# Optimization experiments

Hardware: AMD Instinct MI355X
Metric: run time of the kernel (lower is better)

The kernel has to match this reference:

```python
import jax, jax.numpy as jnp
import numpy as np

H = 4096      # hidden_size
NH = 32       # num_heads
QR = 1536     # q_lora_rank
KVR = 512     # kv_lora_rank
RD = 64       # qk_rope_head_dim
ND = 128      # qk_nope_head_dim
VD = 128      # v_head_dim
QK = RD + ND  # qk_head_dim
EPS = 1e-6
THETA = 10000.0
B, S = 2, 1024


def rmsnorm(x, w):
    # torch: x / (||x|| * d^-0.5 + eps) * w
    norm = jnp.sqrt(jnp.sum(x * x, axis=-1, keepdims=True)) * (x.shape[-1] ** -0.5)
    return x / (norm + EPS) * w


def rope_cos_sin(seq_len):
    inv_freq = 1.0 / (THETA ** (jnp.arange(0, RD, 2, dtype=jnp.float32) / RD))
    t = jnp.arange(seq_len, dtype=jnp.float32)
    freqs = jnp.outer(t, inv_freq)              # [S, RD/2]
    emb = jnp.concatenate([freqs, freqs], -1)   # [S, RD]
    return jnp.cos(emb), jnpp_cos_sin_dummy() if False else jnp.sin(emb)


def rotate_half(x):
    x1, x2 = jnp.split(x, 2, axis=-1)
    return jnp.concatenate([-x2, x1], axis=-1)


def setup_inputs() -> dict:
    key = jax.random.key(0)
    ks = jax.random.split(key, 8)
    sc = 0.02
    return {
        "hidden_states": jax.random.normal(ks[0], (B, S, H), jnp.float32),
        "w_qa": jax.random.normal(ks[1], (H, QR), jnp.float32) * sc,
        "g_qa": jnp.ones((QR,), jnp.float32),
        "w_qb": jax.random.normal(ks[2], (QR, NH * QK), jnp.float32) * sc,
        "w_kva": jax.random.normal(ks[3], (H, KVR + RD), jnp.float32) * sc,
        "g_kva": jnp.ones((KVR,), jnp.float32),
        "w_kvb": jax.random.normal(ks[4], (KVR, NH * (ND + VD)), jnp.float32) * sc,
        "w_o": jax.random.normal(ks[5], (NH * VD, H), jnp.float32) * sc,
    }


def reference(hidden_states, w_qa, g_qa, w_qb, w_kva, g_kva, w_kvb, w_o):
    b, s, _ = hidden_states.shape
    # Q path: LoRA down -> RMSNorm -> LoRA up
    q_c = rmsnorm(hidden_states @ w_qa, g_qa)                       # [b,s,QR]
    q = (q_c @ w_qb).reshape(b, s, NH, QK).transpose(0, 2, 1, 3)    # [b,NH,s,QK]
    q_nope, q_rope = q[..., :ND], q[..., ND:]
    # KV path: joint down-proj, split compressed kv and rope key
    kv = hidden_states @ w_kva                                      # [b,s,KVR+RD]
    k_c, k_rope = kv[..., :KVR], kv[..., KVR:]
    k_c = rmsnorm(k_c, g_kva)
    kst = (k_c @ w_kvb).reshape(b, s, NH, ND + VD).transpose(0, 2, 1, 3)
    k_nope, v = kst[..., :ND], kst[..., ND:]                        # [b,NH,s,ND],[b,NH,s,VD]
    # partial RoPE on the rope slice only
    inv_freq = 1.0 / (THETA ** (jnp.arange(0, RD, 2, dtype=jnp.float32) / RD))
    freqs = jnp.outer(jnp.arange(s, dtype=jnp.float32), inv_freq)
    emb = jnp.concatenate([freqs, freqs], -1)                       # [s,RD]
    cos = jnp.cos(emb)[None, None]                                  # [1,1,s,RD]
    sin = jnp.sin(emb)[None, None]
    k_rope = k_rope[:, None]                                        # [b,1,s,RD]
    q_rope = q_rope * cos + rotate_half(q_rope) * sin
    k_rope = k_rope * cos + rotate_half(k_rope) * sin
    k_rope = jnp.broadcast_to(k_rope, (b, NH, s, RD))
    query = jnp.concatenate([q_nope, q_rope], -1)                   # [b,NH,s,QK]
    key_s = jnp.concatenate([k_nope, k_rope], -1)
    scaling = QK ** -0.5
    scores = jnp.einsum("bhqd,bhkd->bhqk", query, key_s) * scaling  # [b,NH,s,s]
    attn = jax.nn.softmax(scores, axis=-1)
    out = jnp.einsum("bhqk,bhkd->bhqd", attn, v)                    # [b,NH,s,VD]
    out = out.transpose(0, 2, 1, 3).reshape(b, s, NH * VD)
    return out @ w_o                                                # [b,s,H]
```

## Files before the change

### kernel.cpp

```cpp
#include <hip/hip_runtime.h>
#include <hip/hip_bf16.h>
#include <stdint.h>
#include <string.h>

typedef float f32x4_t __attribute__((ext_vector_type(4)));
typedef short s16x8_t __attribute__((ext_vector_type(8)));

#define LDS_AS __attribute__((address_space(3)))
#define GLB_AS __attribute__((address_space(1)))

__device__ __forceinline__ void gload16(void* lds, const void* g) {
    __builtin_amdgcn_global_load_lds((const GLB_AS uint32_t*)g,
                                     (LDS_AS uint32_t*)lds, 16, 0, 0);
}

__device__ __forceinline__ uint32_t pack_bf16(float lo, float hi) {
    union { __hip_bfloat16 h; uint16_t u; } a, b;
    a.h = __float2bfloat16(lo); b.h = __float2bfloat16(hi);
    return (uint32_t)a.u | ((uint32_t)b.u << 16);
}

__global__ __launch_bounds__(256) void rope_table_kernel(float* __restrict__ cos_t,
                                                         float* __restrict__ sin_t) {
    int idx = blockIdx.x * 256 + threadIdx.x;
    int s = idx >> 6, j = idx & 63;
    float invf = powf(10000.0f, -((float)((j & 31) * 2)) / 64.0f);
    float a = (float)s * invf;
    cos_t[idx] = cosf(a);
    sin_t[idx] = sinf(a);
}

__global__ __launch_bounds__(256) void f32_to_bf16_kernel(const float* __restrict__ in,
                                                          __hip_bfloat16* __restrict__ out, int n4) {
    int i = blockIdx.x * 256 + threadIdx.x;
    if (i >= n4) return;
    float4 v = reinterpret_cast<const float4*>(in)[i];
    struct __align__(8) BF4 { __hip_bfloat16 a, b, c, d; } r;
    r.a = __float2bfloat16(v.x); r.b = __float2bfloat16(v.y);
    r.c = __float2bfloat16(v.z); r.d = __float2bfloat16(v.w);
    reinterpret_cast<BF4*>(out)[i] = r;
}

__global__ __launch_bounds__(256) void transpose_convert(const float* __restrict__ W,
                                                         __hip_bfloat16* __restrict__ WT,
                                                         int K, int N, int Npad, float scale) {
    __shared__ float tile[32][33];
    int k0 = blockIdx.y * 32, n0 = blockIdx.x * 32;
    int tx = threadIdx.x & 31, ty = threadIdx.x >> 5;
#pragma unroll
    for (int i = 0; i < 4; i++) {
        int ky = i * 8 + ty;
        int n = n0 + tx;
        float v = 0.f;
        if (n < N) v = W[(size_t)(k0 + ky) * N + n];
        tile[ky][tx] = v;
    }
    __syncthreads();
#pragma unroll
    for (int i = 0; i < 4; i++) {
        int ny = i * 8 + ty;
        WT[(size_t)(n0 + ny) * K + k0 + tx] = __float2bfloat16(tile[tx][ny] * scale);
    }
}

__global__ __launch_bounds__(256) void rmsnorm_kernel(const float* __restrict__ in,
                                                      const float* __restrict__ g,
                                                      __hip_bfloat16* __restrict__ out,
                                                      int cols, int in_stride) {
    int row = blockIdx.x;
    const float* x = in + (size_t)row * in_stride;
    float ss = 0.f;
    for (int c = threadIdx.x; c < cols; c += 256) { float v = x[c]; ss += v * v; }
#pragma unroll
    for (int off = 32; off > 0; off >>= 1) ss += __shfl_xor(ss, off);
    __shared__ float red[4];
    if ((threadIdx.x & 63) == 0) red[threadIdx.x >> 6] = ss;
    __syncthreads();
    float tot = red[0] + red[1] + red[2] + red[3];
    float rms = sqrtf(tot / (float)cols);
    float inv = 1.0f / (rms + 1e-6f);
    for (int c = threadIdx.x; c < cols; c += 256)
        out[(size_t)row * cols + c] = __float2bfloat16(x[c] * inv * g[c]);
}

__global__ __launch_bounds__(256) void rope_k_kernel(const float* __restrict__ kv,
                                                     const float* __restrict__ cos_t,
                                                     const float* __restrict__ sin_t,
                                                     __hip_bfloat16* __restrict__ k_rope) {
    int idx = blockIdx.x * 256 + threadIdx.x;
    int tok = idx >> 5, j = idx & 31;
    int s = tok & 1023;
    const float* x = kv + (size_t)tok * 640 + 512;
    float x1 = x[j], x2 = x[j + 32];
    float co = cos_t[s * 64 + j], si = sin_t[s * 64 + j];
    __hip_bfloat16* o = k_rope + (size_t)tok * 64;
    o[j]      = __float2bfloat16(x1 * co - x2 * si);
    o[j + 32] = __float2bfloat16(x2 * co + x1 * si);
}

__global__ __launch_bounds__(256) void rope_q_kernel(__hip_bfloat16* __restrict__ q,
                                                     const float* __restrict__ cos_t,
                                                     const float* __restrict__ sin_t) {
    int tok = blockIdx.x;
    int s = tok & 1023;
    __hip_bfloat16* row = q + (size_t)tok * 6144;
#pragma unroll
    for (int it = 0; it < 4; it++) {
        int i = it * 256 + threadIdx.x;
        int h = i >> 5, j = i & 31;
        int c = h * 192 + 128 + j;
        float x1 = __bfloat162float(row[c]), x2 = __bfloat162float(row[c + 32]);
        float co = cos_t[s * 64 + j], si = sin_t[s * 64 + j];
        row[c]      = __float2bfloat16(x1 * co - x2 * si);
        row[c + 32] = __float2bfloat16(x2 * co + x1 * si);
    }
}

__global__ __launch_bounds__(256) void transpose_v_kernel(const __hip_bfloat16* __restrict__ kst,
                                                          __hip_bfloat16* __restrict__ V_T) {
    __shared__ __hip_bfloat16 t[64][136];
    int bid = blockIdx.x;
    int st = bid & 15, bh = bid >> 4;
    int h = bh & 31, b = bh >> 5;
    int s0 = st * 64;
#pragma unroll
    for (int i = 0; i < 4; i++) {
        int c = i * 256 + threadIdx.x;
        int r = c >> 4, oct = c & 15;
        *(s16x8_t*)&t[r][oct * 8] =
            *(const s16x8_t*)&kst[(size_t)(b * 1024 + s0 + r) * 8192 + h * 256 + 128 + oct * 8];
    }
    __syncthreads();
#pragma unroll
    for (int i = 0; i < 4; i++) {
        int c = i * 256 + threadIdx.x;
        int vd = c >> 3, oct = c & 7;
        s16x8_t pk;
#pragma unroll
        for (int e = 0; e < 8; e++) pk[e] = *(const short*)&t[oct * 8 + e][vd];
        *(s16x8_t*)&V_T[((size_t)bh * 128 + vd) * 1024 + s0 + oct * 8] = pk;
    }
}

template <int MODE>
__global__ __launch_bounds__(256, 2) void gemm_bt_128(const __hip_bfloat16* __restrict__ A,
                                                      const __hip_bfloat16* __restrict__ BT,
                                                      void* __restrict__ Cout, void* __restrict__ C1,
                                                      int M, int N, int K, int N0, int N1) {
    __shared__ __hip_bfloat16 As[128 * 64];
    __shared__ __hip_bfloat16 Bs[128 * 64];
    const int tid = threadIdx.x;
    const int l = tid & 63, w = tid >> 6;
    const int wr = w >> 1, wc = w & 1;
    const int m0 = blockIdx.y * 128, n0 = blockIdx.x * 128;
    const int lrow = l & 15, lkg = l >> 4;

    f32x4_t acc[4][4];
#pragma unroll
    for (int i = 0; i < 4; i++)
#pragma unroll
        for (int j = 0; j < 4; j++) acc[i][j] = (f32x4_t){0.f, 0.f, 0.f, 0.f};

    for (int k0 = 0; k0 < K; k0 += 64) {
        __syncthreads();
#pragma unroll
        for (int i = 0; i < 4; i++) {
            int s = i * 256 + tid;
            int row = s >> 3, po = s & 7;
            int lo = po ^ (row & 7);
            gload16(&As[s * 8], &A[(size_t)(m0 + row) * K + k0 + lo * 8]);
            gload16(&Bs[s * 8], &BT[(size_t)(n0 + row) * K + k0 + lo * 8]);
        }
        __syncthreads();
#pragma unroll
        for (int ks = 0; ks < 2; ks++) {
            s16x8_t a[4], b[4];
#pragma unroll
            for (int m = 0; m < 4; m++) {
                int row = wr * 64 + m * 16 + lrow;
                int oct = (ks * 4 + lkg) ^ (row & 7);
                a[m] = *(const s16x8_t*)&As[row * 64 + oct * 8];
            }
#pragma unroll
            for (int n = 0; n < 4; n++) {
                int row = wc * 64 + n * 16 + lrow;
                int oct = (ks * 4 + lkg) ^ (row & 7);
                b[n] = *(const s16x8_t*)&Bs[row * 64 + oct * 8];
            }
#pragma unroll
            for (int m = 0; m < 4; m++)
#pragma unroll
                for (int n = 0; n < 4; n++)
                    acc[m][n] = __builtin_amdgcn_mfma_f32_16x16x32_bf16(a[m], b[n], acc[m][n], 0, 0, 0);
        }
    }
#pragma unroll
    for (int m = 0; m < 4; m++) {
        int row = m0 + wr * 64 + m * 16 + lkg * 4;
#pragma unroll
        for (int n = 0; n < 4; n++) {
            int col = n0 + wc * 64 + n * 16 + lrow;
#pragma unroll
            for (int r = 0; r < 4; r++) {
                float v = acc[m][n][r];
                if (MODE == 1) {
                    ((__hip_bfloat16*)Cout)[(size_t)(row + r) * N + col] = __float2bfloat16(v);
                } else if (MODE == 0) {
                    ((float*)Cout)[(size_t)(row + r) * N + col] = v;
                } else {
                    if (col < N0) ((float*)Cout)[(size_t)(row + r) * N0 + col] = v;
                    else          ((float*)C1)[(size_t)(row + r) * N1 + (col - N0)] = v;
                }
            }
        }
    }
}

__global__ __launch_bounds__(256, 3) void attn8_kernel(const __hip_bfloat16* __restrict__ q,
                                                       const __hip_bfloat16* __restrict__ kst,
                                                       const __hip_bfloat16* __restrict__ k_rope,
                                                       const __hip_bfloat16* __restrict__ V_T,
                                                       __hip_bfloat16* __restrict__ attn_out) {
    __shared__ __align__(16) __hip_bfloat16 Ks[2][64 * 192];

    int i = blockIdx.x;
    int bh = (i & 7) * 8 + ((i >> 3) & 7);
    int qt = i >> 6;
    int h = bh & 31, b = bh >> 5;
    int q0 = qt * 64;
    int tid = threadIdx.x, l = tid & 63, w = tid >> 6;
    int lrow = l & 15, lkg = l >> 4;

    s16x8_t qa[6];
    {
        size_t qbase = (size_t)(b * 1024 + q0 + w * 16 + lrow) * 6144 + h * 192;
#pragma unroll
        for (int f = 0; f < 6; f++)
            qa[f] = *(const s16x8_t*)&q[qbase + f * 32 + lkg * 8];
    }
    f32x4_t acc_o[8];
#pragma unroll
    for (int n = 0; n < 8; n++) acc_o[n] = (f32x4_t){0.f, 0.f, 0.f, 0.f};
    float m_run = -1e30f, l_run = 0.f;

    size_t krow_base = (size_t)(b * 1024) * 8192 + h * 256;
    size_t rrow_base = (size_t)(b * 1024) * 64;
    const __hip_bfloat16* vbase = V_T + (size_t)bh * 128 * 1024 + (size_t)lrow * 1024 + lkg * 8;

    auto stage_k = [&](int kv0, int buf) {
#pragma unroll
        for (int it = 0; it < 6; it++) {
            int s = it * 256 + tid;
            int row = s / 24, po = s - row * 24;
            int lo = po ^ (row & 7);
            const __hip_bfloat16* src = (lo < 16)
                ? &kst[krow_base + (size_t)(kv0 + row) * 8192 + lo * 8]
                : &k_rope[rrow_base + (size_t)(kv0 + row) * 64 + (lo - 16) * 8];
            gload16(&Ks[buf][s * 8], src);
        }
    };

    stage_k(0, 0);
    asm volatile("s_waitcnt vmcnt(0)" ::: "memory");
    __syncthreads();

    const int src0 = lrow + ((lkg & 1) << 5);
    const int src1 = src0 + 16;
    const bool hiC = (lkg >> 1) != 0;

    int cur = 0;
    for (int kt = 0; kt < 16; kt++) {
        int kv0 = kt * 64;

        if (kt < 15) stage_k(kv0 + 64, cur ^ 1);

        f32x4_t sc[4];
#pragma unroll
        for (int c = 0; c < 4; c++) sc[c] = (f32x4_t){0.f, 0.f, 0.f, 0.f};
        __builtin_amdgcn_s_setprio(1);
#pragma unroll
        for (int c = 0; c < 4; c++) {
            int row = c * 16 + lrow;
#pragma unroll
            for (int f = 0; f < 6; f++) {
                int po = ((f * 4 + lkg) ^ (lrow & 7)) * 8;
                s16x8_t kb = *(const s16x8_t*)&Ks[cur][row * 192 + po];
                sc[c] = __builtin_amdgcn_mfma_f32_16x16x32_bf16(kb, qa[f], sc[c], 0, 0, 0);
            }
        }
        __builtin_amdgcn_s_setprio(0);

        s16x8_t vb0[8];
#pragma unroll
        for (int n = 0; n < 8; n++)
            vb0[n] = *(const s16x8_t*)&vbase[(size_t)(n * 16) * 1024 + kv0];
        __builtin_amdgcn_sched_barrier(0);

        float mx = sc[0][0];
#pragma unroll
        for (int c = 0; c < 4; c++)
#pragma unroll
            for (int r = 0; r < 4; r++) mx = fmaxf(mx, sc[c][r]);
        mx = fmaxf(mx, __shfl_xor(mx, 16));
        mx = fmaxf(mx, __shfl_xor(mx, 32));
        if (!__all(mx - m_run <= 8.0f)) {
            float mn = fmaxf(m_run, mx);
            float al = __expf(m_run - mn);
            m_run = mn;
            l_run *= al;
#pragma unroll
            for (int n = 0; n < 8; n++) acc_o[n] *= al;
        }
        uint32_t u[4][2];
        float sum = 0.f;
#pragma unroll
        for (int c = 0; c < 4; c++) {
            float p0 = __expf(sc[c][0] - m_run), p1 = __expf(sc[c][1] - m_run);
            float p2 = __expf(sc[c][2] - m_run), p3 = __expf(sc[c][3] - m_run);
            sum += (p0 + p1) + (p2 + p3);
            u[c][0] = pack_bf16(p0, p1);
            u[c][1] = pack_bf16(p2, p3);
        }
        sum += __shfl_xor(sum, 16);
        sum += __shfl_xor(sum, 32);
        l_run += sum;

        {
            uint32_t a0 = __shfl((int)u[0][0], src0), b0 = __shfl((int)u[1][0], src0);
            uint32_t a1 = __shfl((int)u[0][1], src0), b1 = __shfl((int)u[1][1], src0);
            uint32_t a2 = __shfl((int)u[0][0], src1), b2 = __shfl((int)u[1][0], src1);
            uint32_t a3 = __shfl((int)u[0][1], src1), b3 = __shfl((int)u[1][1], src1);
            union { uint32_t wd[4]; s16x8_t v; } pb;
            pb.wd[0] = hiC ? b0 : a0;
            pb.wd[1] = hiC ? b1 : a1;
            pb.wd[2] = hiC ? b2 : a2;
            pb.wd[3] = hiC ? b3 : a3;
            __builtin_amdgcn_s_setprio(1);
#pragma unroll
            for (int n = 0; n < 8; n++)
                acc_o[n] = __builtin_amdgcn_mfma_f32_16x16x32_bf16(vb0[n], pb.v, acc_o[n], 0, 0, 0);
            __builtin_amdgcn_s_setprio(0);
        }
        s16x8_t vb1[8];
#pragma unroll
        for (int n = 0; n < 8; n++)
            vb1[n] = *(const s16x8_t*)&vbase[(size_t)(n * 16) * 1024 + kv0 + 32];
        {
            uint32_t a0 = __shfl((int)u[2][0], src0), b0 = __shfl((int)u[3][0], src0);
            uint32_t a1 = __shfl((int)u[2][1], src0), b1 = __shfl((int)u[3][1], src0);
            uint32_t a2 = __shfl((int)u[2][0], src1), b2 = __shfl((int)u[3][0], src1);
            uint32_t a3 = __shfl((int)u[2][1], src1), b3 = __shfl((int)u[3][1], src1);
            union { uint32_t wd[4]; s16x8_t v; } pb;
            pb.wd[0] = hiC ? b0 : a0;
            pb.wd[1] = hiC ? b1 : a1;
            pb.wd[2] = hiC ? b2 : a2;
            pb.wd[3] = hiC ? b3 : a3;
            __builtin_amdgcn_s_setprio(1);
#pragma unroll
            for (int n = 0; n < 8; n++)
                acc_o[n] = __builtin_amdgcn_mfma_f32_16x16x32_bf16(vb1[n], pb.v, acc_o[n], 0, 0, 0);
            __builtin_amdgcn_s_setprio(0);
        }

        asm volatile("s_waitcnt vmcnt(0)" ::: "memory");
        __syncthreads();
        cur ^= 1;
    }

    float inv = 1.0f / l_run;
    __hip_bfloat16* Ob = &Ks[0][0] + (size_t)w * (16 * 136);
#pragma unroll
    for (int n = 0; n < 8; n++) {
        uint32_t lo = pack_bf16(acc_o[n][0] * inv, acc_o[n][1] * inv);
        uint32_t hi = pack_bf16(acc_o[n][2] * inv, acc_o[n][3] * inv);
        uint32_t* dst = (uint32_t*)&Ob[lrow * 136 + n * 16 + lkg * 4];
        dst[0] = lo;
        dst[1] = hi;
    }
    asm volatile("s_waitcnt lgkmcnt(0)" ::: "memory");
    __builtin_amdgcn_sched_barrier(0);
#pragma unroll
    for (int it = 0; it < 4; it++) {
        int tr = it * 4 + lkg;
        s16x8_t ov = *(const s16x8_t*)&Ob[tr * 136 + lrow * 8];
        *(s16x8_t*)&attn_out[(size_t)(b * 1024 + q0 + w * 16 + tr) * 4096 + h * 128 + lrow * 8] = ov;
    }
}

extern "C" void kernel_launch(void* const* d_in, const int* in_sizes, int n_in,
                              void* d_out, int out_size, void* d_ws, size_t ws_size,
                              hipStream_t stream) {
    const float* hidden = (const float*)d_in[0];
    const float* w_qa   = (const float*)d_in[1];
    const float* g_qa   = (const float*)d_in[2];
    const float* w_qb   = (const float*)d_in[3];
    const float* w_kva  = (const float*)d_in[4];
    const float* g_kva  = (const float*)d_in[5];
    const float* w_kvb  = (const float*)d_in[6];
    const float* w_o    = (const float*)d_in[7];
    float* out = (float*)d_out;

    char* base = (char*)d_ws;
    size_t off = 0;
    auto alloc = [&](size_t bytes) -> void* {
        off = (off + 255) & ~(size_t)255;
        void* p = base + off;
        off += bytes;
        return p;
    };
    float* cos_t = (float*)alloc(1024 * 64 * 4);
    float* sin_t = (float*)alloc(1024 * 64 * 4);
    __hip_bfloat16* hid_b  = (__hip_bfloat16*)alloc(2048ull * 4096 * 2);
    __hip_bfloat16* wqaT   = (__hip_bfloat16*)alloc(1536ull * 4096 * 2);
    __hip_bfloat16* wkvaT  = (__hip_bfloat16*)alloc(640ull * 4096 * 2);
    __hip_bfloat16* wqbT   = (__hip_bfloat16*)alloc(6144ull * 1536 * 2);
    __hip_bfloat16* wkvbT  = (__hip_bfloat16*)alloc(8192ull * 512 * 2);
    __hip_bfloat16* woT    = (__hip_bfloat16*)alloc(4096ull * 4096 * 2);
    float* q_a             = (float*)alloc(2048ull * 1536 * 4);
    __hip_bfloat16* q_c    = (__hip_bfloat16*)alloc(2048ull * 1536 * 2);
    __hip_bfloat16* q_buf  = (__hip_bfloat16*)alloc(2048ull * 6144 * 2);
    float* kv              = (float*)alloc(2048ull * 640 * 4);
    __hip_bfloat16* k_c    = (__hip_bfloat16*)alloc(2048ull * 512 * 2);
    __hip_bfloat16* k_rope = (__hip_bfloat16*)alloc(2048ull * 64 * 2);
    __hip_bfloat16* kst    = (__hip_bfloat16*)alloc(2048ull * 8192 * 2);
    __hip_bfloat16* V_T      = hid_b;
    __hip_bfloat16* attn_out = wqbT;

    const float qscale = 0.07216878364870323f;

    rope_table_kernel<<<256, 256, 0, stream>>>(cos_t, sin_t);
    f32_to_bf16_kernel<<<8192, 256, 0, stream>>>(hidden, hid_b, 2048 * 4096 / 4);
    transpose_convert<<<dim3(1536 / 32, 4096 / 32), 256, 0, stream>>>(w_qa, wqaT, 4096, 1536, 1536, 1.0f);
    transpose_convert<<<dim3(640 / 32, 4096 / 32), 256, 0, stream>>>(w_kva, wkvaT, 4096, 576, 640, 1.0f);
    transpose_convert<<<dim3(6144 / 32, 1536 / 32), 256, 0, stream>>>(w_qb, wqbT, 1536, 6144, 6144, qscale);
    transpose_convert<<<dim3(8192 / 32, 512 / 32), 256, 0, stream>>>(w_kvb, wkvbT, 512, 8192, 8192, 1.0f);
    transpose_convert<<<dim3(4096 / 32, 4096 / 32), 256, 0, stream>>>(w_o, woT, 4096, 4096, 4096, 1.0f);

    gemm_bt_128<2><<<dim3(17, 16), 256, 0, stream>>>(hid_b, wqaT, q_a, kv, 2048, 2176, 4096, 1536, 640);
    rmsnorm_kernel<<<2048, 256, 0, stream>>>(q_a, g_qa, q_c, 1536, 1536);
    rmsnorm_kernel<<<2048, 256, 0, stream>>>(kv, g_kva, k_c, 512, 640);
    rope_k_kernel<<<2048 * 32 / 256, 256, 0, stream>>>(kv, cos_t, sin_t, k_rope);
    gemm_bt_128<1><<<dim3(6144 / 128, 16), 256, 0, stream>>>(q_c, wqbT, q_buf, nullptr, 2048, 6144, 1536, 0, 0);
    rope_q_kernel<<<2048, 256, 0, stream>>>(q_buf, cos_t, sin_t);
    gemm_bt_128<1><<<dim3(8192 / 128, 16), 256, 0, stream>>>(k_c, wkvbT, kst, nullptr, 2048, 8192, 512, 0, 0);
    transpose_v_kernel<<<1024, 256, 0, stream>>>(kst, V_T);
    attn8_kernel<<<1024, 256, 0, stream>>>(q_buf, kst, k_rope, V_T, attn_out);
    gemm_bt_128<0><<<dim3(4096 / 128, 16), 256, 0, stream>>>(attn_out, woT, out, nullptr, 2048, 4096, 4096, 0, 0);
}
```

Baseline: 465.9 us.

## Vectorize weight transpose, split rope-key staging in attention, raise occupancy hints

The weight transpose-convert kernel now reads float4 rows over 128-wide tiles and writes 8 bf16 values per store, which cuts the number of memory transactions. The attention kernel double-buffers only the nope part of K. The rope-key part goes into a single-buffered LDS tile that is reloaded after an extra barrier, which lowers LDS use so four blocks can fit per CU. The GEMM launch bounds rise to 3 blocks per CU, which may force register spills. The added barrier and single-buffered rope load may stall the attention loop.

```diff
diff --git a/kernel.cpp b/kernel.cpp
--- a/kernel.cpp
+++ b/kernel.cpp
@@ -1,7 +1,6 @@
 #include <hip/hip_runtime.h>
 #include <hip/hip_bf16.h>
 #include <stdint.h>
-#include <string.h>
 
 typedef float f32x4_t __attribute__((ext_vector_type(4)));
 typedef short s16x8_t __attribute__((ext_vector_type(8)));
@@ -44,22 +43,38 @@
 __global__ __launch_bounds__(256) void transpose_convert(const float* __restrict__ W,
                                                          __hip_bfloat16* __restrict__ WT,
                                                          int K, int N, int Npad, float scale) {
-    __shared__ float tile[32][33];
-    int k0 = blockIdx.y * 32, n0 = blockIdx.x * 32;
+    __shared__ float tile[32][132];
+    int k0 = blockIdx.y * 32, n0 = blockIdx.x * 128;
     int tx = threadIdx.x & 31, ty = threadIdx.x >> 5;
 #pragma unroll
     for (int i = 0; i < 4; i++) {
         int ky = i * 8 + ty;
-        int n = n0 + tx;
-        float v = 0.f;
-        if (n < N) v = W[(size_t)(k0 + ky) * N + n];
-        tile[ky][tx] = v;
+        int n = n0 + tx * 4;
+        float4 v;
+        if (n + 3 < N) {
+            v = *(const float4*)&W[(size_t)(k0 + ky) * N + n];
+        } else {
+            float t0 = (n + 0 < N) ? W[(size_t)(k0 + ky) * N + n + 0] : 0.f;
+            float t1 = (n + 1 < N) ? W[(size_t)(k0 + ky) * N + n + 1] : 0.f;
+            float t2 = (n + 2 < N) ? W[(size_t)(k0 + ky) * N + n + 2] : 0.f;
+            float t3 = (n + 3 < N) ? W[(size_t)(k0 + ky) * N + n + 3] : 0.f;
+            v = make_float4(t0, t1, t2, t3);
+        }
+        *(float4*)&tile[ky][tx * 4] = v;
     }
     __syncthreads();
-#pragma unroll
-    for (int i = 0; i < 4; i++) {
-        int ny = i * 8 + ty;
-        WT[(size_t)(n0 + ny) * K + k0 + tx] = __float2bfloat16(tile[tx][ny] * scale);
+    int ny = threadIdx.x & 127, kh = threadIdx.x >> 7;
+#pragma unroll
+    for (int oct = 0; oct < 2; oct++) {
+        int kb = kh * 16 + oct * 8;
+        union { short s[8]; s16x8_t v; } pk;
+#pragma unroll
+        for (int e = 0; e < 8; e++) {
+            union { __hip_bfloat16 h; short s; } cv;
+            cv.h = __float2bfloat16(tile[kb + e][ny] * scale);
+            pk.s[e] = cv.s;
+        }
+        *(s16x8_t*)&WT[(size_t)(n0 + ny) * K + k0 + kb] = pk.v;
     }
 }
 
@@ -143,7 +158,7 @@
 }
 
 template <int MODE>
-__global__ __launch_bounds__(256, 2) void gemm_bt_128(const __hip_bfloat16* __restrict__ A,
+__global__ __launch_bounds__(256, 3) void gemm_bt_128(const __hip_bfloat16* __restrict__ A,
                                                       const __hip_bfloat16* __restrict__ BT,
                                                       void* __restrict__ Cout, void* __restrict__ C1,
                                                       int M, int N, int K, int N0, int N1) {
@@ -216,12 +231,13 @@
     }
 }
 
-__global__ __launch_bounds__(256, 3) void attn8_kernel(const __hip_bfloat16* __restrict__ q,
+__global__ __launch_bounds__(256, 4) void attn9_kernel(const __hip_bfloat16* __restrict__ q,
                                                        const __hip_bfloat16* __restrict__ kst,
                                                        const __hip_bfloat16* __restrict__ k_rope,
                                                        const __hip_bfloat16* __restrict__ V_T,
                                                        __hip_bfloat16* __restrict__ attn_out) {
-    __shared__ __align__(16) __hip_bfloat16 Ks[2][64 * 192];
+    __shared__ __align__(16) __hip_bfloat16 Ks[2][64 * 128];
+    __shared__ __align__(16) __hip_bfloat16 Kr[64 * 64];
 
     int i = blockIdx.x;
     int bh = (i & 7) * 8 + ((i >> 3) & 7);
@@ -247,20 +263,27 @@
     size_t rrow_base = (size_t)(b * 1024) * 64;
     const __hip_bfloat16* vbase = V_T + (size_t)bh * 128 * 1024 + (size_t)lrow * 1024 + lkg * 8;
 
-    auto stage_k = [&](int kv0, int buf) {
-#pragma unroll
-        for (int it = 0; it < 6; it++) {
+    auto stage_nope = [&](int kv0, int buf) {
+#pragma unroll
+        for (int it = 0; it < 4; it++) {
             int s = it * 256 + tid;
-            int row = s / 24, po = s - row * 24;
+            int row = s >> 4, po = s & 15;
             int lo = po ^ (row & 7);
-            const __hip_bfloat16* src = (lo < 16)
-                ? &kst[krow_base + (size_t)(kv0 + row) * 8192 + lo * 8]
-                : &k_rope[rrow_base + (size_t)(kv0 + row) * 64 + (lo - 16) * 8];
-            gload16(&Ks[buf][s * 8], src);
+            gload16(&Ks[buf][s * 8], &kst[krow_base + (size_t)(kv0 + row) * 8192 + lo * 8]);
         }
     };
-
-    stage_k(0, 0);
+    auto stage_rope = [&](int kv0) {
+#pragma unroll
+        for (int it = 0; it < 2; it++) {
+            int s = it * 256 + tid;
+            int row = s >> 3, po = s & 7;
+            int lo = po ^ (row & 7);
+            gload16(&Kr[s * 8], &k_rope[rrow_base + (size_t)(kv0 + row) * 64 + lo * 8]);
+        }
+    };
+
+    stage_nope(0, 0);
+    stage_rope(0);
     asm volatile("s_waitcnt vmcnt(0)" ::: "memory");
     __syncthreads();
 
@@ -272,7 +295,7 @@
     for (int kt = 0; kt < 16; kt++) {
         int kv0 = kt * 64;
 
-        if (kt < 15) stage_k(kv0 + 64, cur ^ 1);
+        if (kt < 15) stage_nope(kv0 + 64, cur ^ 1);
 
         f32x4_t sc[4];
 #pragma unroll
@@ -282,13 +305,28 @@
         for (int c = 0; c < 4; c++) {
             int row = c * 16 + lrow;
 #pragma unroll
-            for (int f = 0; f < 6; f++) {
-                int po = ((f * 4 + lkg) ^ (lrow & 7)) * 8;
-                s16x8_t kb = *(const s16x8_t*)&Ks[cur][row * 192 + po];
+            for (int f = 0; f < 4; f++) {
+                int po = ((f * 4 + lkg) ^ (row & 7)) * 8;
+                s16x8_t kb = *(const s16x8_t*)&Ks[cur][row * 128 + po];
                 sc[c] = __builtin_amdgcn_mfma_f32_16x16x32_bf16(kb, qa[f], sc[c], 0, 0, 0);
             }
         }
+#pragma unroll
+        for (int c = 0; c < 4; c++) {
+            int row = c * 16 + lrow;
+#pragma unroll
+            for (int f = 4; f < 6; f++) {
+                int po = (((f - 4) * 4 + lkg) ^ (row & 7)) * 8;
+                s16x8_t kb = *(const s16x8_t*)&Kr[row * 64 + po];
+                sc[c] = __builtin_amdgcn_mfma_f32_16x16x32_bf16(kb, qa[f], sc[c], 0, 0, 0);
+            }
+        }
         __builtin_amdgcn_s_setprio(0);
+
+        asm volatile("s_waitcnt lgkmcnt(0)" ::: "memory");
+        __builtin_amdgcn_sched_barrier(0);
+        __builtin_amdgcn_s_barrier();
+        if (kt < 15) stage_rope(kv0 + 64);
 
         s16x8_t vb0[8];
 #pragma unroll
@@ -430,11 +468,11 @@
 
     rope_table_kernel<<<256, 256, 0, stream>>>(cos_t, sin_t);
     f32_to_bf16_kernel<<<8192, 256, 0, stream>>>(hidden, hid_b, 2048 * 4096 / 4);
-    transpose_convert<<<dim3(1536 / 32, 4096 / 32), 256, 0, stream>>>(w_qa, wqaT, 4096, 1536, 1536, 1.0f);
-    transpose_convert<<<dim3(640 / 32, 4096 / 32), 256, 0, stream>>>(w_kva, wkvaT, 4096, 576, 640, 1.0f);
-    transpose_convert<<<dim3(6144 / 32, 1536 / 32), 256, 0, stream>>>(w_qb, wqbT, 1536, 6144, 6144, qscale);
-    transpose_convert<<<dim3(8192 / 32, 512 / 32), 256, 0, stream>>>(w_kvb, wkvbT, 512, 8192, 8192, 1.0f);
-    transpose_convert<<<dim3(4096 / 32, 4096 / 32), 256, 0, stream>>>(w_o, woT, 4096, 4096, 4096, 1.0f);
+    transpose_convert<<<dim3(1536 / 128, 4096 / 32), 256, 0, stream>>>(w_qa, wqaT, 4096, 1536, 1536, 1.0f);
+    transpose_convert<<<dim3(640 / 128, 4096 / 32), 256, 0, stream>>>(w_kva, wkvaT, 4096, 576, 640, 1.0f);
+    transpose_convert<<<dim3(6144 / 128, 1536 / 32), 256, 0, stream>>>(w_qb, wqbT, 1536, 6144, 6144, qscale);
+    transpose_convert<<<dim3(8192 / 128, 512 / 32), 256, 0, stream>>>(w_kvb, wkvbT, 512, 8192, 8192, 1.0f);
+    transpose_convert<<<dim3(4096 / 128, 4096 / 32), 256, 0, stream>>>(w_o, woT, 4096, 4096, 4096, 1.0f);
 
     gemm_bt_128<2><<<dim3(17, 16), 256, 0, stream>>>(hid_b, wqaT, q_a, kv, 2048, 2176, 4096, 1536, 640);
     rmsnorm_kernel<<<2048, 256, 0, stream>>>(q_a, g_qa, q_c, 1536, 1536);
@@ -444,6 +482,6 @@
     rope_q_kernel<<<2048, 256, 0, stream>>>(q_buf, cos_t, sin_t);
     gemm_bt_128<1><<<dim3(8192 / 128, 16), 256, 0, stream>>>(k_c, wkvbT, kst, nullptr, 2048, 8192, 512, 0, 0);
     transpose_v_kernel<<<1024, 256, 0, stream>>>(kst, V_T);
-    attn8_kernel<<<1024, 256, 0, stream>>>(q_buf, kst, k_rope, V_T, attn_out);
+    attn9_kernel<<<1024, 256, 0, stream>>>(q_buf, kst, k_rope, V_T, attn_out);
     gemm_bt_128<0><<<dim3(4096 / 128, 16), 256, 0, stream>>>(attn_out, woT, out, nullptr, 2048, 4096, 4096, 0, 0);
 }
```

New measurement: 487.5 us. 1.05x slower.
